# Kernel optimization log

Measured on AMD Instinct MI355X. Metric: run time of the kernel, lower is better.

The kernel has to match this reference:

```python
import jax, jax.numpy as jnp
import numpy as np

N_NODES = 100000
N_EDGES = 1600000
D_IN, D_HID, D_OUT = 64, 64, 32


def setup_inputs() -> dict:
    key = jax.random.key(0)
    ks = jax.random.split(key, 9)
    x = jax.random.normal(ks[0], (N_NODES, D_IN), dtype=jnp.float32)
    edge_index = jax.random.randint(ks[1], (2, N_EDGES), 0, N_NODES, dtype=jnp.int64)
    s1 = 1.0 / np.sqrt(D_IN)
    s2 = 1.0 / np.sqrt(D_HID)
    return {
        "x": x,
        "edge_index": edge_index,
        # layer 1: lin_l (aggregated neighbors, has bias), lin_r (root, no bias)
        "W1_l": jax.random.uniform(ks[2], (D_IN, D_HID), jnp.float32, -s1, s1),
        "b1": jax.random.uniform(ks[3], (D_HID,), jnp.float32, -s1, s1),
        "W1_r": jax.random.uniform(ks[4], (D_IN, D_HID), jnp.float32, -s1, s1),
        # layer 2
        "W2_l": jax.random.uniform(ks[5], (D_HID, D_OUT), jnp.float32, -s2, s2),
        "b2": jax.random.uniform(ks[6], (D_OUT,), jnp.float32, -s2, s2),
        "W2_r": jax.random.uniform(ks[7], (D_HID, D_OUT), jnp.float32, -s2, s2),
    }


def _sage_conv(x, src, dst, W_l, b_l, W_r, n_nodes):
    """PyG SAGEConv with mean aggregation:
       out_i = W_l @ mean_{j in N(i)} x_j + b_l + W_r @ x_i
    """
    msgs = x[src]  # [E, d] gather of source-node features
    summed = jax.ops.segment_sum(msgs, dst, num_segments=n_nodes)  # [N, d]
    deg = jax.ops.segment_sum(jnp.ones((src.shape[0],), x.dtype), dst, num_segments=n_nodes)
    mean = summed / jnp.maximum(deg, 1.0)[:, None]
    return mean @ W_l + b_l + x @ W_r


def reference(x, edge_index, W1_l, b1, W1_r, W2_l, b2, W2_r):
    src, dst = edge_index[0], edge_index[1]
    n = x.shape[0]
    h = _sage_conv(x, src, dst, W1_l, b1, W1_r, n)
    h = jax.nn.relu(h)
    out = _sage_conv(h, src, dst, W2_l, b2, W2_r, n)
    return out
```

## Files before the change

kernel.cpp:

```cpp
#include <hip/hip_runtime.h>


typedef __attribute__((ext_vector_type(4))) float f4;
typedef __attribute__((ext_vector_type(2))) float f2;
typedef __attribute__((ext_vector_type(4))) unsigned short us4;
typedef __attribute__((ext_vector_type(8))) unsigned short us8;
typedef __attribute__((ext_vector_type(8))) short bfrag;

#define BSHIFT 9
#define BSZ (1 << BSHIFT)
#define NBMAX 256
#define NBLK 512
#define LSTR 72

static __device__ inline unsigned short f2bf(float f) {
    union { float f; unsigned u; } v; v.f = f;
    unsigned u = v.u;
    u = (u + 0x7FFFu + ((u >> 16) & 1u)) >> 16;
    return (unsigned short)u;
}
static __device__ inline float bf2f(unsigned short h) {
    union { unsigned u; float f; } v; v.u = ((unsigned)h) << 16; return v.f;
}

__global__ __launch_bounds__(256) void k_bhist(const int* __restrict__ dst, int E, int chunk,
                                               int NB, int* __restrict__ cntmat) {
    __shared__ int hist[NBMAX];
    int t = threadIdx.x;
    hist[t] = 0;
    __syncthreads();
    int lo = blockIdx.x * chunk, hi = min(lo + chunk, E);
    for (int e = lo + t; e < hi; e += 256) atomicAdd(&hist[dst[e] >> BSHIFT], 1);
    __syncthreads();
    if (t < NB) cntmat[blockIdx.x * NB + t] = hist[t];
}

__global__ __launch_bounds__(256) void k_cscan(int* __restrict__ cntmat, int NB,
                                               int* __restrict__ btot) {
    __shared__ int wt[4];
    int b = blockIdx.x;
    int t = threadIdx.x;
    int v0 = cntmat[(2 * t) * NB + b];
    int v1 = cntmat[(2 * t + 1) * NB + b];
    int tsum = v0 + v1;
    int lane = t & 63, w = t >> 6;
    int p = tsum;
    for (int off = 1; off < 64; off <<= 1) { int u = __shfl_up(p, off); if (lane >= off) p += u; }
    if (lane == 63) wt[w] = p;
    __syncthreads();
    int wb = 0;
    for (int i = 0; i < w; i++) wb += wt[i];
    int excl = wb + p - tsum;
    cntmat[(2 * t) * NB + b] = excl;
    cntmat[(2 * t + 1) * NB + b] = excl + v0;
    if (t == 255) btot[b] = wb + p;
}

__global__ __launch_bounds__(256) void k_bscan(const int* __restrict__ btot, int NB, int E, int N,
                                               int* __restrict__ bucket_base,
                                               int* __restrict__ row_off) {
    __shared__ int wt[4];
    int t = threadIdx.x;
    int v = (t < NB) ? btot[t] : 0;
    int lane = t & 63, w = t >> 6;
    int p = v;
    for (int off = 1; off < 64; off <<= 1) { int u = __shfl_up(p, off); if (lane >= off) p += u; }
    if (lane == 63) wt[w] = p;
    __syncthreads();
    int wb = 0;
    for (int i = 0; i < w; i++) wb += wt[i];
    int incl = wb + p;
    int excl = incl - v;
    if (t < NB) bucket_base[t] = excl;
    if (t == NB - 1) bucket_base[NB] = incl;
    if (t == 0) row_off[N] = E;
}

__global__ __launch_bounds__(256) void k_bscatter(const int* __restrict__ src, const int* __restrict__ dst,
                                                  int E, int chunk, int NB,
                                                  const int* __restrict__ bucket_base,
                                                  const int* __restrict__ cntmat,
                                                  unsigned int* __restrict__ bdata) {
    __shared__ int lbase[NBMAX], lcur[NBMAX];
    int t = threadIdx.x;
    if (t < NB) { lbase[t] = bucket_base[t] + cntmat[blockIdx.x * NB + t]; lcur[t] = 0; }
    __syncthreads();
    int lo = blockIdx.x * chunk, hi = min(lo + chunk, E);
    for (int e = lo + t; e < hi; e += 256) {
        int d = dst[e];
        int b = d >> BSHIFT;
        int pos = lbase[b] + atomicAdd(&lcur[b], 1);
        bdata[pos] = ((unsigned)(d & (BSZ - 1)) << 17) | (unsigned)src[e];
    }
}

__global__ __launch_bounds__(256) void k_bucket_csr(const unsigned int* __restrict__ bdata,
                                                    const int* __restrict__ bucket_base,
                                                    int N, int* __restrict__ row_off,
                                                    int* __restrict__ col_src) {
    __shared__ int fh[BSZ];
    __shared__ int wtot[4];
    int t = threadIdx.x;
    int b = blockIdx.x;
    int ebase = bucket_base[b], eend = bucket_base[b + 1];
    fh[2 * t] = 0; fh[2 * t + 1] = 0;
    __syncthreads();
    for (int i = ebase + t; i < eend; i += 256) atomicAdd(&fh[bdata[i] >> 17], 1);
    __syncthreads();
    int a0 = fh[2 * t], a1 = fh[2 * t + 1];
    int psum = a0 + a1;
    int lane = t & 63, w = t >> 6;
    int v = psum;
    for (int off = 1; off < 64; off <<= 1) { int u = __shfl_up(v, off); if (lane >= off) v += u; }
    if (lane == 63) wtot[w] = v;
    __syncthreads();
    int wbase = 0;
    for (int i = 0; i < w; i++) wbase += wtot[i];
    int excl = wbase + v - psum;
    int e0 = excl, e1 = excl + a0;
    int n0 = (b << BSHIFT) + 2 * t, n1 = n0 + 1;
    if (n0 < N) row_off[n0] = ebase + e0;
    if (n1 < N) row_off[n1] = ebase + e1;
    fh[2 * t] = e0; fh[2 * t + 1] = e1;
    __syncthreads();
    for (int i = ebase + t; i < eend; i += 256) {
        unsigned vv = bdata[i];
        int dl = vv >> 17;
        int pos = atomicAdd(&fh[dl], 1);
        col_src[ebase + pos] = (int)(vv & 0x1FFFFu);
    }
}

__global__ __launch_bounds__(256) void k_gemm1(const float* __restrict__ x,
                                               const float* __restrict__ Wl,
                                               const float* __restrict__ Wr, int N,
                                               unsigned char* __restrict__ t1l8,
                                               unsigned short* __restrict__ t1rb) {
    __shared__ unsigned short sX[64 * LSTR];
    __shared__ unsigned short sW[128 * LSTR];
    int t = threadIdx.x;
    int r0 = blockIdx.x * 64;
    for (int i = t; i < 2048; i += 256) {
        int which = i >> 10;
        int rem = i & 1023;
        int k = rem >> 4;
        int c4 = (rem & 15) * 4;
        f4 v = *(const f4*)&(which ? Wr : Wl)[k * 64 + c4];
        int nb = which * 64 + c4;
        sW[(nb + 0) * LSTR + k] = f2bf(v[0]);
        sW[(nb + 1) * LSTR + k] = f2bf(v[1]);
        sW[(nb + 2) * LSTR + k] = f2bf(v[2]);
        sW[(nb + 3) * LSTR + k] = f2bf(v[3]);
    }
    {
        int row = t >> 2;
        int q = (t & 3) * 16;
        bool valid = (r0 + row) < N;
#pragma unroll
        for (int j = 0; j < 4; j++) {
            f4 v = {0.f, 0.f, 0.f, 0.f};
            if (valid) v = *(const f4*)&x[(size_t)(r0 + row) * 64 + q + j * 4];
            us4 bv;
            bv[0] = f2bf(v[0]); bv[1] = f2bf(v[1]); bv[2] = f2bf(v[2]); bv[3] = f2bf(v[3]);
            *(us4*)&sX[row * LSTR + q + j * 4] = bv;
        }
    }
    __syncthreads();
    int wv = t >> 6;
    int l  = t & 63;
    int lm = l & 15;
    int lk = (l >> 4) * 8;
    f4 acc[8] = {{0.f,0.f,0.f,0.f},{0.f,0.f,0.f,0.f},{0.f,0.f,0.f,0.f},{0.f,0.f,0.f,0.f},
                 {0.f,0.f,0.f,0.f},{0.f,0.f,0.f,0.f},{0.f,0.f,0.f,0.f},{0.f,0.f,0.f,0.f}};
#pragma unroll
    for (int kh = 0; kh < 2; kh++) {
        bfrag a = *(const bfrag*)&sX[(wv * 16 + lm) * LSTR + kh * 32 + lk];
#pragma unroll
        for (int nt = 0; nt < 8; nt++) {
            bfrag b = *(const bfrag*)&sW[(nt * 16 + lm) * LSTR + kh * 32 + lk];
            acc[nt] = __builtin_amdgcn_mfma_f32_16x16x32_bf16(a, b, acc[nt], 0, 0, 0);
        }
    }
    int orow0 = r0 + wv * 16 + (l >> 4) * 4;
#pragma unroll
    for (int j = 0; j < 4; j++) {
        int rr = orow0 + j;
        if (rr < N) {
#pragma unroll
            for (int nt = 0; nt < 4; nt++) {
                float v = acc[nt][j];
                unsigned w8 = __builtin_amdgcn_cvt_pk_fp8_f32(v, v, 0u, false);
                t1l8[(size_t)rr * 64 + nt * 16 + lm] = (unsigned char)(w8 & 0xFFu);
            }
#pragma unroll
            for (int nt = 0; nt < 4; nt++) {
                t1rb[(size_t)rr * 64 + nt * 16 + lm] = f2bf(acc[nt + 4][j]);
            }
        }
    }
}

__global__ __launch_bounds__(256) void k_gemm2(const unsigned short* __restrict__ hbf,
                                               const float* __restrict__ Wl,
                                               const float* __restrict__ Wr,
                                               const float* __restrict__ b2, int N,
                                               unsigned short* __restrict__ t2l,
                                               float* __restrict__ t2r) {
    __shared__ unsigned short sX[64 * LSTR];
    __shared__ unsigned short sW[64 * LSTR];
    int t = threadIdx.x;
    int r0 = blockIdx.x * 64;
    for (int i = t; i < 1024; i += 256) {
        int which = i >> 9;
        int rem = i & 511;
        int k = rem >> 3;
        int c4 = (rem & 7) * 4;
        f4 v = *(const f4*)&(which ? Wr : Wl)[k * 32 + c4];
        int nb = which * 32 + c4;
        sW[(nb + 0) * LSTR + k] = f2bf(v[0]);
        sW[(nb + 1) * LSTR + k] = f2bf(v[1]);
        sW[(nb + 2) * LSTR + k] = f2bf(v[2]);
        sW[(nb + 3) * LSTR + k] = f2bf(v[3]);
    }
    {
        int row = t >> 2;
        int q = (t & 3) * 16;
        us8 z = {0,0,0,0,0,0,0,0};
        us8 v0 = z, v1 = z;
        if (r0 + row < N) {
            v0 = *(const us8*)&hbf[(size_t)(r0 + row) * 64 + q];
            v1 = *(const us8*)&hbf[(size_t)(r0 + row) * 64 + q + 8];
        }
        *(us8*)&sX[row * LSTR + q] = v0;
        *(us8*)&sX[row * LSTR + q + 8] = v1;
    }
    __syncthreads();
    int wv = t >> 6;
    int l  = t & 63;
    int lm = l & 15;
    int lk = (l >> 4) * 8;
    f4 acc[4] = {{0.f,0.f,0.f,0.f},{0.f,0.f,0.f,0.f},{0.f,0.f,0.f,0.f},{0.f,0.f,0.f,0.f}};
#pragma unroll
    for (int kh = 0; kh < 2; kh++) {
        bfrag a = *(const bfrag*)&sX[(wv * 16 + lm) * LSTR + kh * 32 + lk];
#pragma unroll
        for (int nt = 0; nt < 4; nt++) {
            bfrag b = *(const bfrag*)&sW[(nt * 16 + lm) * LSTR + kh * 32 + lk];
            acc[nt] = __builtin_amdgcn_mfma_f32_16x16x32_bf16(a, b, acc[nt], 0, 0, 0);
        }
    }
    int orow0 = r0 + wv * 16 + (l >> 4) * 4;
#pragma unroll
    for (int j = 0; j < 4; j++) {
        int rr = orow0 + j;
        if (rr < N) {
#pragma unroll
            for (int nt = 0; nt < 2; nt++) {
                t2l[(size_t)rr * 32 + nt * 16 + lm] = f2bf(acc[nt][j]);
            }
#pragma unroll
            for (int nt = 0; nt < 2; nt++) {
                int c = nt * 16 + lm;
                t2r[(size_t)rr * 32 + c] = acc[nt + 2][j] + b2[c];
            }
        }
    }
}

__global__ __launch_bounds__(256) void k_agg1(const unsigned char* __restrict__ t1l8,
                                              const int* __restrict__ row_off,
                                              const int* __restrict__ col_src,
                                              const float* __restrict__ b1,
                                              const unsigned short* __restrict__ t1rb,
                                              int N, unsigned short* __restrict__ hbf) {
    int gid = (blockIdx.x * blockDim.x + threadIdx.x) >> 4;
    int gl  = threadIdx.x & 15;
    if (gid >= N) return;
    int beg = row_off[gid], end = row_off[gid + 1];
    f4 a0 = {0.f,0.f,0.f,0.f}, a1 = {0.f,0.f,0.f,0.f};
    f4 a2 = {0.f,0.f,0.f,0.f}, a3 = {0.f,0.f,0.f,0.f};
    int k = beg;
    for (; k + 7 < end; k += 8) {
        int i0 = col_src[k],     i1 = col_src[k + 1], i2 = col_src[k + 2], i3 = col_src[k + 3];
        int i4 = col_src[k + 4], i5 = col_src[k + 5], i6 = col_src[k + 6], i7 = col_src[k + 7];
        unsigned u0 = *(const unsigned*)&t1l8[(size_t)i0 * 64 + gl * 4];
        unsigned u1 = *(const unsigned*)&t1l8[(size_t)i1 * 64 + gl * 4];
        unsigned u2 = *(const unsigned*)&t1l8[(size_t)i2 * 64 + gl * 4];
        unsigned u3 = *(const unsigned*)&t1l8[(size_t)i3 * 64 + gl * 4];
        unsigned u4 = *(const unsigned*)&t1l8[(size_t)i4 * 64 + gl * 4];
        unsigned u5 = *(const unsigned*)&t1l8[(size_t)i5 * 64 + gl * 4];
        unsigned u6 = *(const unsigned*)&t1l8[(size_t)i6 * 64 + gl * 4];
        unsigned u7 = *(const unsigned*)&t1l8[(size_t)i7 * 64 + gl * 4];
        f2 l0 = __builtin_amdgcn_cvt_pk_f32_fp8(u0, false), h0 = __builtin_amdgcn_cvt_pk_f32_fp8(u0, true);
        f2 l1 = __builtin_amdgcn_cvt_pk_f32_fp8(u1, false), h1 = __builtin_amdgcn_cvt_pk_f32_fp8(u1, true);
        f2 l2 = __builtin_amdgcn_cvt_pk_f32_fp8(u2, false), h2 = __builtin_amdgcn_cvt_pk_f32_fp8(u2, true);
        f2 l3 = __builtin_amdgcn_cvt_pk_f32_fp8(u3, false), h3 = __builtin_amdgcn_cvt_pk_f32_fp8(u3, true);
        f2 l4 = __builtin_amdgcn_cvt_pk_f32_fp8(u4, false), h4 = __builtin_amdgcn_cvt_pk_f32_fp8(u4, true);
        f2 l5 = __builtin_amdgcn_cvt_pk_f32_fp8(u5, false), h5 = __builtin_amdgcn_cvt_pk_f32_fp8(u5, true);
        f2 l6 = __builtin_amdgcn_cvt_pk_f32_fp8(u6, false), h6 = __builtin_amdgcn_cvt_pk_f32_fp8(u6, true);
        f2 l7 = __builtin_amdgcn_cvt_pk_f32_fp8(u7, false), h7 = __builtin_amdgcn_cvt_pk_f32_fp8(u7, true);
        a0[0] += l0[0] + l4[0]; a0[1] += l0[1] + l4[1]; a0[2] += h0[0] + h4[0]; a0[3] += h0[1] + h4[1];
        a1[0] += l1[0] + l5[0]; a1[1] += l1[1] + l5[1]; a1[2] += h1[0] + h5[0]; a1[3] += h1[1] + h5[1];
        a2[0] += l2[0] + l6[0]; a2[1] += l2[1] + l6[1]; a2[2] += h2[0] + h6[0]; a2[3] += h2[1] + h6[1];
        a3[0] += l3[0] + l7[0]; a3[1] += l3[1] + l7[1]; a3[2] += h3[0] + h7[0]; a3[3] += h3[1] + h7[1];
    }
    for (; k + 3 < end; k += 4) {
        int i0 = col_src[k], i1 = col_src[k + 1], i2 = col_src[k + 2], i3 = col_src[k + 3];
        unsigned u0 = *(const unsigned*)&t1l8[(size_t)i0 * 64 + gl * 4];
        unsigned u1 = *(const unsigned*)&t1l8[(size_t)i1 * 64 + gl * 4];
        unsigned u2 = *(const unsigned*)&t1l8[(size_t)i2 * 64 + gl * 4];
        unsigned u3 = *(const unsigned*)&t1l8[(size_t)i3 * 64 + gl * 4];
        f2 l0 = __builtin_amdgcn_cvt_pk_f32_fp8(u0, false), h0 = __builtin_amdgcn_cvt_pk_f32_fp8(u0, true);
        f2 l1 = __builtin_amdgcn_cvt_pk_f32_fp8(u1, false), h1 = __builtin_amdgcn_cvt_pk_f32_fp8(u1, true);
        f2 l2 = __builtin_amdgcn_cvt_pk_f32_fp8(u2, false), h2 = __builtin_amdgcn_cvt_pk_f32_fp8(u2, true);
        f2 l3 = __builtin_amdgcn_cvt_pk_f32_fp8(u3, false), h3 = __builtin_amdgcn_cvt_pk_f32_fp8(u3, true);
        a0[0] += l0[0]; a0[1] += l0[1]; a0[2] += h0[0]; a0[3] += h0[1];
        a1[0] += l1[0]; a1[1] += l1[1]; a1[2] += h1[0]; a1[3] += h1[1];
        a2[0] += l2[0]; a2[1] += l2[1]; a2[2] += h2[0]; a2[3] += h2[1];
        a3[0] += l3[0]; a3[1] += l3[1]; a3[2] += h3[0]; a3[3] += h3[1];
    }
    for (; k < end; k++) {
        unsigned u0 = *(const unsigned*)&t1l8[(size_t)col_src[k] * 64 + gl * 4];
        f2 l0 = __builtin_amdgcn_cvt_pk_f32_fp8(u0, false), h0 = __builtin_amdgcn_cvt_pk_f32_fp8(u0, true);
        a0[0] += l0[0]; a0[1] += l0[1]; a0[2] += h0[0]; a0[3] += h0[1];
    }
    f4 s = (a0 + a1) + (a2 + a3);
    float deg = (float)(end - beg);
    float inv = deg > 0.f ? 1.f / deg : 0.f;
    us4 rb = *(const us4*)&t1rb[(size_t)gid * 64 + gl * 4];
    f4 bb = *(const f4*)&b1[gl * 4];
    us4 ob;
#pragma unroll
    for (int j = 0; j < 4; j++) {
        float v = s[j] * inv + bf2f(rb[j]) + bb[j];
        ob[j] = f2bf(v > 0.f ? v : 0.f);
    }
    *(us4*)&hbf[(size_t)gid * 64 + gl * 4] = ob;
}

__global__ __launch_bounds__(256) void k_agg2(const unsigned short* __restrict__ t2l,
                                              const float* __restrict__ t2r,
                                              const int* __restrict__ row_off,
                                              const int* __restrict__ col_src,
                                              int N, float* __restrict__ out) {
    int gid = (blockIdx.x * blockDim.x + threadIdx.x) >> 4;
    int gl  = threadIdx.x & 15;
    if (gid >= N) return;
    int beg = row_off[gid], end = row_off[gid + 1];
    f2 a0 = {0.f,0.f}, a1 = {0.f,0.f}, a2 = {0.f,0.f}, a3 = {0.f,0.f};
    int k = beg;
    for (; k + 7 < end; k += 8) {
        int i0 = col_src[k],     i1 = col_src[k + 1], i2 = col_src[k + 2], i3 = col_src[k + 3];
        int i4 = col_src[k + 4], i5 = col_src[k + 5], i6 = col_src[k + 6], i7 = col_src[k + 7];
        unsigned u0 = *(const unsigned*)&t2l[(size_t)i0 * 32 + gl * 2];
        unsigned u1 = *(const unsigned*)&t2l[(size_t)i1 * 32 + gl * 2];
        unsigned u2 = *(const unsigned*)&t2l[(size_t)i2 * 32 + gl * 2];
        unsigned u3 = *(const unsigned*)&t2l[(size_t)i3 * 32 + gl * 2];
        unsigned u4 = *(const unsigned*)&t2l[(size_t)i4 * 32 + gl * 2];
        unsigned u5 = *(const unsigned*)&t2l[(size_t)i5 * 32 + gl * 2];
        unsigned u6 = *(const unsigned*)&t2l[(size_t)i6 * 32 + gl * 2];
        unsigned u7 = *(const unsigned*)&t2l[(size_t)i7 * 32 + gl * 2];
        a0[0] += bf2f((unsigned short)(u0 & 0xFFFFu)) + bf2f((unsigned short)(u4 & 0xFFFFu));
        a0[1] += bf2f((unsigned short)(u0 >> 16))     + bf2f((unsigned short)(u4 >> 16));
        a1[0] += bf2f((unsigned short)(u1 & 0xFFFFu)) + bf2f((unsigned short)(u5 & 0xFFFFu));
        a1[1] += bf2f((unsigned short)(u1 >> 16))     + bf2f((unsigned short)(u5 >> 16));
        a2[0] += bf2f((unsigned short)(u2 & 0xFFFFu)) + bf2f((unsigned short)(u6 & 0xFFFFu));
        a2[1] += bf2f((unsigned short)(u2 >> 16))     + bf2f((unsigned short)(u6 >> 16));
        a3[0] += bf2f((unsigned short)(u3 & 0xFFFFu)) + bf2f((unsigned short)(u7 & 0xFFFFu));
        a3[1] += bf2f((unsigned short)(u3 >> 16))     + bf2f((unsigned short)(u7 >> 16));
    }
    for (; k + 3 < end; k += 4) {
        int i0 = col_src[k], i1 = col_src[k + 1], i2 = col_src[k + 2], i3 = col_src[k + 3];
        unsigned u0 = *(const unsigned*)&t2l[(size_t)i0 * 32 + gl * 2];
        unsigned u1 = *(const unsigned*)&t2l[(size_t)i1 * 32 + gl * 2];
        unsigned u2 = *(const unsigned*)&t2l[(size_t)i2 * 32 + gl * 2];
        unsigned u3 = *(const unsigned*)&t2l[(size_t)i3 * 32 + gl * 2];
        a0[0] += bf2f((unsigned short)(u0 & 0xFFFFu)); a0[1] += bf2f((unsigned short)(u0 >> 16));
        a1[0] += bf2f((unsigned short)(u1 & 0xFFFFu)); a1[1] += bf2f((unsigned short)(u1 >> 16));
        a2[0] += bf2f((unsigned short)(u2 & 0xFFFFu)); a2[1] += bf2f((unsigned short)(u2 >> 16));
        a3[0] += bf2f((unsigned short)(u3 & 0xFFFFu)); a3[1] += bf2f((unsigned short)(u3 >> 16));
    }
    for (; k < end; k++) {
        unsigned u0 = *(const unsigned*)&t2l[(size_t)col_src[k] * 32 + gl * 2];
        a0[0] += bf2f((unsigned short)(u0 & 0xFFFFu)); a0[1] += bf2f((unsigned short)(u0 >> 16));
    }
    f2 s = (a0 + a1) + (a2 + a3);
    float deg = (float)(end - beg);
    float inv = deg > 0.f ? 1.f / deg : 0.f;
    f2 rr = *(const f2*)&t2r[(size_t)gid * 32 + gl * 2];
    f2 o = {s[0] * inv + rr[0], s[1] * inv + rr[1]};
    *(f2*)&out[(size_t)gid * 32 + gl * 2] = o;
}

extern "C" void kernel_launch(void* const* d_in, const int* in_sizes, int n_in,
                              void* d_out, int out_size, void* d_ws, size_t ws_size,
                              hipStream_t stream) {
    const float* x   = (const float*)d_in[0];
    const int*   ei  = (const int*)d_in[1];
    const float* W1l = (const float*)d_in[2];
    const float* b1  = (const float*)d_in[3];
    const float* W1r = (const float*)d_in[4];
    const float* W2l = (const float*)d_in[5];
    const float* b2  = (const float*)d_in[6];
    const float* W2r = (const float*)d_in[7];
    float* out = (float*)d_out;

    int N = in_sizes[0] / 64;
    int E = in_sizes[1] / 2;
    const int* src = ei;
    const int* dst = ei + E;
    int NB = (N + BSZ - 1) >> BSHIFT;

    char* ws = (char*)d_ws;
    size_t off = 0;
    auto alloc = [&](size_t bytes) { void* p = ws + off; off += (bytes + 255) & ~(size_t)255; return p; };
    int* cntmat      = (int*)alloc((size_t)NBLK * NB * 4);
    int* btot        = (int*)alloc((size_t)NB * 4);
    int* bucket_base = (int*)alloc((size_t)(NB + 1) * 4);
    int* row_off     = (int*)alloc((size_t)(N + 1) * 4);
    int* col_src     = (int*)alloc((size_t)E * 4);
    unsigned int* bdata = (unsigned int*)alloc((size_t)E * 4);
    unsigned char* t1l8 = (unsigned char*)alloc((size_t)N * 64);
    unsigned short* t1rb = (unsigned short*)alloc((size_t)N * 64 * 2);
    unsigned short* hbf  = (unsigned short*)alloc((size_t)N * 64 * 2);

    unsigned short* t2l = (unsigned short*)bdata;
    float* t2r          = (float*)t1rb;

    int chunk = (E + NBLK - 1) / NBLK;
    k_bhist<<<NBLK, 256, 0, stream>>>(dst, E, chunk, NB, cntmat);
    k_cscan<<<NB, 256, 0, stream>>>(cntmat, NB, btot);
    k_bscan<<<1, 256, 0, stream>>>(btot, NB, E, N, bucket_base, row_off);
    k_bscatter<<<NBLK, 256, 0, stream>>>(src, dst, E, chunk, NB, bucket_base, cntmat, bdata);
    k_bucket_csr<<<NB, 256, 0, stream>>>(bdata, bucket_base, N, row_off, col_src);

    int gb = (N + 63) / 64;
    k_gemm1<<<gb, 256, 0, stream>>>(x, W1l, W1r, N, t1l8, t1rb);
    k_agg1<<<((size_t)N * 16 + 255) / 256, 256, 0, stream>>>(t1l8, row_off, col_src, b1, t1rb, N, hbf);
    k_gemm2<<<gb, 256, 0, stream>>>(hbf, W2l, W2r, b2, N, t2l, t2r);
    k_agg2<<<((size_t)N * 16 + 255) / 256, 256, 0, stream>>>(t2l, t2r, row_off, col_src, N, out);
}
```

Before: 134.7 us.

## Fuse histogram into first GEMM launch and fold bucket scan into consumers

```diff
diff --git a/kernel.cpp b/kernel.cpp
--- a/kernel.cpp
+++ b/kernel.cpp
@@ -23,122 +23,28 @@
     union { unsigned u; float f; } v; v.u = ((unsigned)h) << 16; return v.f;
 }
 
-__global__ __launch_bounds__(256) void k_bhist(const int* __restrict__ dst, int E, int chunk,
-                                               int NB, int* __restrict__ cntmat) {
-    __shared__ int hist[NBMAX];
+__global__ __launch_bounds__(256) void k_g1h(const float* __restrict__ x,
+                                             const float* __restrict__ Wl,
+                                             const float* __restrict__ Wr, int N, int gb,
+                                             unsigned char* __restrict__ t1l8,
+                                             unsigned short* __restrict__ t1rb,
+                                             const int* __restrict__ dst, int E, int chunk,
+                                             int NB, int* __restrict__ cntmat) {
+    __shared__ unsigned short smem[64 * LSTR + 128 * LSTR];
     int t = threadIdx.x;
-    hist[t] = 0;
-    __syncthreads();
-    int lo = blockIdx.x * chunk, hi = min(lo + chunk, E);
-    for (int e = lo + t; e < hi; e += 256) atomicAdd(&hist[dst[e] >> BSHIFT], 1);
-    __syncthreads();
-    if (t < NB) cntmat[blockIdx.x * NB + t] = hist[t];
-}
-
-__global__ __launch_bounds__(256) void k_cscan(int* __restrict__ cntmat, int NB,
-                                               int* __restrict__ btot) {
-    __shared__ int wt[4];
-    int b = blockIdx.x;
-    int t = threadIdx.x;
-    int v0 = cntmat[(2 * t) * NB + b];
-    int v1 = cntmat[(2 * t + 1) * NB + b];
-    int tsum = v0 + v1;
-    int lane = t & 63, w = t >> 6;
-    int p = tsum;
-    for (int off = 1; off < 64; off <<= 1) { int u = __shfl_up(p, off); if (lane >= off) p += u; }
-    if (lane == 63) wt[w] = p;
-    __syncthreads();
-    int wb = 0;
-    for (int i = 0; i < w; i++) wb += wt[i];
-    int excl = wb + p - tsum;
-    cntmat[(2 * t) * NB + b] = excl;
-    cntmat[(2 * t + 1) * NB + b] = excl + v0;
-    if (t == 255) btot[b] = wb + p;
-}
-
-__global__ __launch_bounds__(256) void k_bscan(const int* __restrict__ btot, int NB, int E, int N,
-                                               int* __restrict__ bucket_base,
-                                               int* __restrict__ row_off) {
-    __shared__ int wt[4];
-    int t = threadIdx.x;
-    int v = (t < NB) ? btot[t] : 0;
-    int lane = t & 63, w = t >> 6;
-    int p = v;
-    for (int off = 1; off < 64; off <<= 1) { int u = __shfl_up(p, off); if (lane >= off) p += u; }
-    if (lane == 63) wt[w] = p;
-    __syncthreads();
-    int wb = 0;
-    for (int i = 0; i < w; i++) wb += wt[i];
-    int incl = wb + p;
-    int excl = incl - v;
-    if (t < NB) bucket_base[t] = excl;
-    if (t == NB - 1) bucket_base[NB] = incl;
-    if (t == 0) row_off[N] = E;
-}
-
-__global__ __launch_bounds__(256) void k_bscatter(const int* __restrict__ src, const int* __restrict__ dst,
-                                                  int E, int chunk, int NB,
-                                                  const int* __restrict__ bucket_base,
-                                                  const int* __restrict__ cntmat,
-                                                  unsigned int* __restrict__ bdata) {
-    __shared__ int lbase[NBMAX], lcur[NBMAX];
-    int t = threadIdx.x;
-    if (t < NB) { lbase[t] = bucket_base[t] + cntmat[blockIdx.x * NB + t]; lcur[t] = 0; }
-    __syncthreads();
-    int lo = blockIdx.x * chunk, hi = min(lo + chunk, E);
-    for (int e = lo + t; e < hi; e += 256) {
-        int d = dst[e];
-        int b = d >> BSHIFT;
-        int pos = lbase[b] + atomicAdd(&lcur[b], 1);
-        bdata[pos] = ((unsigned)(d & (BSZ - 1)) << 17) | (unsigned)src[e];
-    }
-}
-
-__global__ __launch_bounds__(256) void k_bucket_csr(const unsigned int* __restrict__ bdata,
-                                                    const int* __restrict__ bucket_base,
-                                                    int N, int* __restrict__ row_off,
-                                                    int* __restrict__ col_src) {
-    __shared__ int fh[BSZ];
-    __shared__ int wtot[4];
-    int t = threadIdx.x;
-    int b = blockIdx.x;
-    int ebase = bucket_base[b], eend = bucket_base[b + 1];
-    fh[2 * t] = 0; fh[2 * t + 1] = 0;
-    __syncthreads();
-    for (int i = ebase + t; i < eend; i += 256) atomicAdd(&fh[bdata[i] >> 17], 1);
-    __syncthreads();
-    int a0 = fh[2 * t], a1 = fh[2 * t + 1];
-    int psum = a0 + a1;
-    int lane = t & 63, w = t >> 6;
-    int v = psum;
-    for (int off = 1; off < 64; off <<= 1) { int u = __shfl_up(v, off); if (lane >= off) v += u; }
-    if (lane == 63) wtot[w] = v;
-    __syncthreads();
-    int wbase = 0;
-    for (int i = 0; i < w; i++) wbase += wtot[i];
-    int excl = wbase + v - psum;
-    int e0 = excl, e1 = excl + a0;
-    int n0 = (b << BSHIFT) + 2 * t, n1 = n0 + 1;
-    if (n0 < N) row_off[n0] = ebase + e0;
-    if (n1 < N) row_off[n1] = ebase + e1;
-    fh[2 * t] = e0; fh[2 * t + 1] = e1;
-    __syncthreads();
-    for (int i = ebase + t; i < eend; i += 256) {
-        unsigned vv = bdata[i];
-        int dl = vv >> 17;
-        int pos = atomicAdd(&fh[dl], 1);
-        col_src[ebase + pos] = (int)(vv & 0x1FFFFu);
-    }
-}
-
-__global__ __launch_bounds__(256) void k_gemm1(const float* __restrict__ x,
-                                               const float* __restrict__ Wl,
-                                               const float* __restrict__ Wr, int N,
-                                               unsigned char* __restrict__ t1l8,
-                                               unsigned short* __restrict__ t1rb) {
-    __shared__ unsigned short sX[64 * LSTR];
-    __shared__ unsigned short sW[128 * LSTR];
-    int t = threadIdx.x;
+    if ((int)blockIdx.x >= gb) {
+        int* hist = (int*)smem;
+        hist[t] = 0;
+        __syncthreads();
+        int bb = blockIdx.x - gb;
+        int lo = bb * chunk, hi = min(lo + chunk, E);
+        for (int e = lo + t; e < hi; e += 256) atomicAdd(&hist[dst[e] >> BSHIFT], 1);
+        __syncthreads();
+        if (t < NB) cntmat[bb * NB + t] = hist[t];
+        return;
+    }
+    unsigned short* sX = smem;
+    unsigned short* sW = smem + 64 * LSTR;
     int r0 = blockIdx.x * 64;
     for (int i = t; i < 2048; i += 256) {
         int which = i >> 10;
@@ -197,6 +103,106 @@
                 t1rb[(size_t)rr * 64 + nt * 16 + lm] = f2bf(acc[nt + 4][j]);
             }
         }
+    }
+}
+
+__global__ __launch_bounds__(256) void k_cscan(int* __restrict__ cntmat, int NB, int E, int N,
+                                               int* __restrict__ btot, int* __restrict__ row_off) {
+    __shared__ int wt[4];
+    int b = blockIdx.x;
+    int t = threadIdx.x;
+    int v0 = cntmat[(2 * t) * NB + b];
+    int v1 = cntmat[(2 * t + 1) * NB + b];
+    int tsum = v0 + v1;
+    int lane = t & 63, w = t >> 6;
+    int p = tsum;
+    for (int off = 1; off < 64; off <<= 1) { int u = __shfl_up(p, off); if (lane >= off) p += u; }
+    if (lane == 63) wt[w] = p;
+    __syncthreads();
+    int wb = 0;
+    for (int i = 0; i < w; i++) wb += wt[i];
+    int excl = wb + p - tsum;
+    cntmat[(2 * t) * NB + b] = excl;
+    cntmat[(2 * t + 1) * NB + b] = excl + v0;
+    if (t == 255) btot[b] = wb + p;
+    if (b == 0 && t == 0) row_off[N] = E;
+}
+
+__global__ __launch_bounds__(256) void k_bscatter(const int* __restrict__ src, const int* __restrict__ dst,
+                                                  int E, int chunk, int NB,
+                                                  const int* __restrict__ btot,
+                                                  const int* __restrict__ cntmat,
+                                                  unsigned int* __restrict__ bdata) {
+    __shared__ int lbase[NBMAX], lcur[NBMAX];
+    __shared__ int wt[4];
+    int t = threadIdx.x;
+    int v = (t < NB) ? btot[t] : 0;
+    int lane = t & 63, w = t >> 6;
+    int p = v;
+    for (int off = 1; off < 64; off <<= 1) { int u = __shfl_up(p, off); if (lane >= off) p += u; }
+    if (lane == 63) wt[w] = p;
+    __syncthreads();
+    int wb = 0;
+    for (int i = 0; i < w; i++) wb += wt[i];
+    int excl = wb + p - v;
+    if (t < NB) { lbase[t] = excl + cntmat[blockIdx.x * NB + t]; lcur[t] = 0; }
+    __syncthreads();
+    int lo = blockIdx.x * chunk, hi = min(lo + chunk, E);
+    for (int e = lo + t; e < hi; e += 256) {
+        int d = dst[e];
+        int b = d >> BSHIFT;
+        int pos = lbase[b] + atomicAdd(&lcur[b], 1);
+        bdata[pos] = ((unsigned)(d & (BSZ - 1)) << 17) | (unsigned)src[e];
+    }
+}
+
+__global__ __launch_bounds__(256) void k_bucket_csr(const unsigned int* __restrict__ bdata,
+                                                    const int* __restrict__ btot, int NB,
+                                                    int N, int* __restrict__ row_off,
+                                                    int* __restrict__ col_src) {
+    __shared__ int fh[BSZ];
+    __shared__ int wt1[4], wt2[4];
+    __shared__ int sb[2];
+    int t = threadIdx.x;
+    int b = blockIdx.x;
+    {
+        int v = (t < NB) ? btot[t] : 0;
+        int lane = t & 63, w = t >> 6;
+        int p = v;
+        for (int off = 1; off < 64; off <<= 1) { int u = __shfl_up(p, off); if (lane >= off) p += u; }
+        if (lane == 63) wt1[w] = p;
+        __syncthreads();
+        int wb = 0;
+        for (int i = 0; i < w; i++) wb += wt1[i];
+        int excl = wb + p - v;
+        if (t == b) { sb[0] = excl; sb[1] = excl + v; }
+    }
+    fh[2 * t] = 0; fh[2 * t + 1] = 0;
+    __syncthreads();
+    int ebase = sb[0], eend = sb[1];
+    for (int i = ebase + t; i < eend; i += 256) atomicAdd(&fh[bdata[i] >> 17], 1);
+    __syncthreads();
+    int a0 = fh[2 * t], a1 = fh[2 * t + 1];
+    int psum = a0 + a1;
+    int lane = t & 63, w = t >> 6;
+    int v = psum;
+    for (int off = 1; off < 64; off <<= 1) { int u = __shfl_up(v, off); if (lane >= off) v += u; }
+    if (lane == 63) wt2[w] = v;
+    __syncthreads();
+    int wbase = 0;
+    for (int i = 0; i < w; i++) wbase += wt2[i];
+    int excl = wbase + v - psum;
+    int e0 = excl, e1 = excl + a0;
+    int n0 = (b << BSHIFT) + 2 * t, n1 = n0 + 1;
+    if (n0 < N) row_off[n0] = ebase + e0;
+    if (n1 < N) row_off[n1] = ebase + e1;
+    fh[2 * t] = e0; fh[2 * t + 1] = e1;
+    __syncthreads();
+    for (int i = ebase + t; i < eend; i += 256) {
+        unsigned vv = bdata[i];
+        int dl = vv >> 17;
+        int pos = atomicAdd(&fh[dl], 1);
+        col_src[ebase + pos] = (int)(vv & 0x1FFFFu);
     }
 }
 
@@ -416,7 +422,6 @@
     auto alloc = [&](size_t bytes) { void* p = ws + off; off += (bytes + 255) & ~(size_t)255; return p; };
     int* cntmat      = (int*)alloc((size_t)NBLK * NB * 4);
     int* btot        = (int*)alloc((size_t)NB * 4);
-    int* bucket_base = (int*)alloc((size_t)(NB + 1) * 4);
     int* row_off     = (int*)alloc((size_t)(N + 1) * 4);
     int* col_src     = (int*)alloc((size_t)E * 4);
     unsigned int* bdata = (unsigned int*)alloc((size_t)E * 4);
@@ -428,14 +433,14 @@
     float* t2r          = (float*)t1rb;
 
     int chunk = (E + NBLK - 1) / NBLK;
-    k_bhist<<<NBLK, 256, 0, stream>>>(dst, E, chunk, NB, cntmat);
-    k_cscan<<<NB, 256, 0, stream>>>(cntmat, NB, btot);
-    k_bscan<<<1, 256, 0, stream>>>(btot, NB, E, N, bucket_base, row_off);
-    k_bscatter<<<NBLK, 256, 0, stream>>>(src, dst, E, chunk, NB, bucket_base, cntmat, bdata);
-    k_bucket_csr<<<NB, 256, 0, stream>>>(bdata, bucket_base, N, row_off, col_src);
-
     int gb = (N + 63) / 64;
-    k_gemm1<<<gb, 256, 0, stream>>>(x, W1l, W1r, N, t1l8, t1rb);
+
+    k_g1h<<<gb + NBLK, 256, 0, stream>>>(x, W1l, W1r, N, gb, t1l8, t1rb,
+                                         dst, E, chunk, NB, cntmat);
+    k_cscan<<<NB, 256, 0, stream>>>(cntmat, NB, E, N, btot, row_off);
+    k_bscatter<<<NBLK, 256, 0, stream>>>(src, dst, E, chunk, NB, btot, cntmat, bdata);
+    k_bucket_csr<<<NB, 256, 0, stream>>>(bdata, btot, NB, N, row_off, col_src);
+
     k_agg1<<<((size_t)N * 16 + 255) / 256, 256, 0, stream>>>(t1l8, row_off, col_src, b1, t1rb, N, hbf);
     k_gemm2<<<gb, 256, 0, stream>>>(hbf, W2l, W2r, b2, N, t2l, t2r);
     k_agg2<<<((size_t)N * 16 + 255) / 256, 256, 0, stream>>>(t2l, t2r, row_off, col_src, N, out);
```

Result: faster. 129.5 us (median of 2 runs) (-3.9%).
